# Optimization experiments

Measured on AMD Instinct MI355X. Metric: run time of the kernel, lower is better.

Reference implementation:

```python
import jax, jax.numpy as jnp
import numpy as np

B, N, M, K = 4, 2048, 8192, 3          # batches, coarse pts/batch, fine pts/batch, knn k
C_IN, C_SKIP, H, C_OUT = 256, 128, 256, 128


def setup_inputs() -> dict:
    key = jax.random.key(0)
    ks = jax.random.split(key, 8)
    x = jax.random.normal(ks[0], (B * N, C_IN), jnp.float32)
    pos = jax.random.normal(ks[1], (B * N, 3), jnp.float32)
    batch = jnp.repeat(jnp.arange(B, dtype=jnp.int64), N)        # sorted, equal-sized batches
    x_skip = jax.random.normal(ks[2], (B * M, C_SKIP), jnp.float32)
    pos_skip = jax.random.normal(ks[3], (B * M, 3), jnp.float32)
    batch_skip = jnp.repeat(jnp.arange(B, dtype=jnp.int64), M)
    # MLP params: Linear(384->256) + ReLU + Linear(256->128)
    W1 = jax.random.normal(ks[4], (C_IN + C_SKIP, H), jnp.float32) / np.sqrt(C_IN + C_SKIP)
    b1 = jnp.zeros((H,), jnp.float32)
    W2 = jax.random.normal(ks[5], (H, C_OUT), jnp.float32) / np.sqrt(H)
    b2 = jnp.zeros((C_OUT,), jnp.float32)
    return {"x": x, "pos": pos, "x_skip": x_skip, "pos_skip": pos_skip,
            "W1": W1, "b1": b1, "W2": W2, "b2": b2,
            "batch": batch, "batch_skip": batch_skip}


def _knn_interpolate(x, pos, pos_skip):
    # x: [B*N, C], pos: [B*N, 3], pos_skip: [B*M, 3]; batches are equal-sized & sorted,
    # so per-batch kNN == reshape to [B, n, ...] (matches batch/batch_skip vectors).
    xb = x.reshape(B, N, C_IN)
    pb = pos.reshape(B, N, 3)
    qb = pos_skip.reshape(B, M, 3)
    # squared pairwise distances via GEMM expansion: [B, M, N]
    d2 = (jnp.sum(qb * qb, -1)[:, :, None]
          + jnp.sum(pb * pb, -1)[:, None, :]
          - 2.0 * jnp.einsum('bmd,bnd->bmn', qb, pb))
    neg_d2, idx = jax.lax.top_k(-d2, K)           # k smallest distances
    d2k = jnp.maximum(-neg_d2, 0.0)               # [B, M, K]
    w = 1.0 / (d2k + 1e-16)                       # inverse-squared-distance weights
    feats = xb[jnp.arange(B)[:, None, None], idx] # gather: [B, M, K, C]
    interp = jnp.sum(w[..., None] * feats, axis=2) / jnp.sum(w, axis=2)[..., None]
    return interp.reshape(B * M, C_IN)


def reference(x, pos, x_skip, pos_skip, W1, b1, W2, b2, batch, batch_skip):
    xi = _knn_interpolate(x, pos, pos_skip)              # [B*M, C_IN]
    h = jnp.concatenate([xi, x_skip], axis=1)            # [B*M, C_IN+C_SKIP]
    h = jax.nn.relu(h @ W1 + b1)
    out = h @ W2 + b2                                    # [B*M, C_OUT]
    return (out, pos_skip, batch_skip)
```

## Files before the change

kernel.cpp:

```cpp
#include <hip/hip_runtime.h>
#include <math.h>
#include <stdint.h>

#define Bn    4
#define Nn    2048
#define Mn    8192
#define CIN   256
#define CSKIP 128
#define HID   256
#define COUT  128
#define KTOT  384

typedef short bf16x8 __attribute__((ext_vector_type(8)));
typedef float f32x16 __attribute__((ext_vector_type(16)));

__device__ __forceinline__ ushort f2bf(float f) {
    union { float f; unsigned u; } v; v.f = f;
    return (ushort)((v.u + 0x7fffu + ((v.u >> 16) & 1u)) >> 16);
}

__global__ __launch_bounds__(256) void fused_front(
    const float* __restrict__ x,
    const float* __restrict__ pos,
    const float* __restrict__ xs,
    const float* __restrict__ pos_skip,
    const float* __restrict__ W1, const float* __restrict__ W2,
    ushort* __restrict__ Abig,
    ushort* __restrict__ W1T, ushort* __restrict__ W2T,
    float* __restrict__ tail_dst)
{
    __shared__ float4 spos[Nn];
    __shared__ float  sPd[8][3][33];
    __shared__ int    sPi[8][3][33];
    __shared__ int    sIdx[32][3];
    __shared__ float  sW[32][4];

    const int bid = blockIdx.x;
    const int tid = threadIdx.x;

    if (bid >= 1024) {
        const int cb = bid - 1024;
        if (cb < 4096) {
            const int q   = cb * 256 + tid;
            const int row = q >> 5;
            const int cq  = (q & 31) * 4;
            const float4 v = *(const float4*)(xs + (size_t)row * CSKIP + cq);
            ushort4 o; o.x = f2bf(v.x); o.y = f2bf(v.y); o.z = f2bf(v.z); o.w = f2bf(v.w);
            *(ushort4*)(Abig + (size_t)row * KTOT + CIN + cq) = o;
        } else if (cb < 4192) {
            const int q  = (cb - 4096) * 256 + tid;
            const int n  = q / 96;
            const int kq = (q % 96) * 4;
            ushort4 o;
            o.x = f2bf(W1[(size_t)(kq + 0) * HID + n]);
            o.y = f2bf(W1[(size_t)(kq + 1) * HID + n]);
            o.z = f2bf(W1[(size_t)(kq + 2) * HID + n]);
            o.w = f2bf(W1[(size_t)(kq + 3) * HID + n]);
            *(ushort4*)(W1T + (size_t)n * KTOT + kq) = o;
        } else if (cb < 4224) {
            const int q  = (cb - 4192) * 256 + tid;
            const int n  = q >> 6;
            const int kq = (q & 63) * 4;
            ushort4 o;
            o.x = f2bf(W2[(size_t)(kq + 0) * COUT + n]);
            o.y = f2bf(W2[(size_t)(kq + 1) * COUT + n]);
            o.z = f2bf(W2[(size_t)(kq + 2) * COUT + n]);
            o.w = f2bf(W2[(size_t)(kq + 3) * COUT + n]);
            *(ushort4*)(W2T + (size_t)n * HID + kq) = o;
        } else {
            const int i = (cb - 4224) * 256 + tid;
            const int nPos = Bn * Mn * 3;
            if (i < nPos) tail_dst[i] = pos_skip[i];
            else          tail_dst[i] = (float)((i - nPos) >> 13);
        }
        return;
    }

    const int qloc   = tid & 31;
    const int chunk  = tid >> 5;
    const int blockQ = bid * 32;
    const int b      = blockQ / Mn;

    for (int i = tid; i < Nn; i += 256) {
        const float* p = pos + (size_t)(b * Nn + i) * 3;
        float p0 = p[0], p1 = p[1], p2 = p[2];
        float pp = __fadd_rn(__fadd_rn(__fmul_rn(p0, p0), __fmul_rn(p1, p1)),
                             __fmul_rn(p2, p2));
        spos[i] = make_float4(2.0f * p0, 2.0f * p1, 2.0f * p2, pp);
    }
    __syncthreads();

    const int q = blockQ + qloc;
    const float* qp = pos_skip + (size_t)q * 3;
    const float q0 = qp[0], q1 = qp[1], q2 = qp[2];
    const float qq = __fadd_rn(__fadd_rn(__fmul_rn(q0, q0), __fmul_rn(q1, q1)),
                               __fmul_rn(q2, q2));

    float dA = INFINITY, dB = INFINITY, dC = INFINITY;
    int   iA = 0, iB = 0, iC = 0;
    const int base = chunk * 256;
#pragma unroll 8
    for (int j = 0; j < 256; ++j) {
        const float4 P = spos[base + j];
        const float dot2 = __fadd_rn(__fadd_rn(__fmul_rn(q0, P.x), __fmul_rn(q1, P.y)),
                                     __fmul_rn(q2, P.z));
        const float d = __fsub_rn(__fadd_rn(qq, P.w), dot2);
        const int idx = base + j;
        const bool c1 = d < dA, c2 = d < dB, c3 = d < dC;
        dC = c3 ? (c2 ? dB : d) : dC;  iC = c3 ? (c2 ? iB : idx) : iC;
        dB = c2 ? (c1 ? dA : d) : dB;  iB = c2 ? (c1 ? iA : idx) : iB;
        dA = c1 ? d : dA;              iA = c1 ? idx : iA;
    }
    sPd[chunk][0][qloc] = dA; sPd[chunk][1][qloc] = dB; sPd[chunk][2][qloc] = dC;
    sPi[chunk][0][qloc] = iA; sPi[chunk][1][qloc] = iB; sPi[chunk][2][qloc] = iC;
    __syncthreads();

    if (tid < 32) {
        float mA = INFINITY, mB = INFINITY, mC = INFINITY;
        int   jA = 0, jB = 0, jC = 0;
#pragma unroll
        for (int c = 0; c < 8; ++c) {
#pragma unroll
            for (int s = 0; s < 3; ++s) {
                const float d = sPd[c][s][tid];
                const int   i = sPi[c][s][tid];
                const bool c1 = d < mA, c2 = d < mB, c3 = d < mC;
                mC = c3 ? (c2 ? mB : d) : mC;  jC = c3 ? (c2 ? jB : i) : jC;
                mB = c2 ? (c1 ? mA : d) : mB;  jB = c2 ? (c1 ? jA : i) : jB;
                mA = c1 ? d : mA;              jA = c1 ? i : jA;
            }
        }
        const float w0 = 1.0f / (fmaxf(mA, 0.0f) + 1e-16f);
        const float w1 = 1.0f / (fmaxf(mB, 0.0f) + 1e-16f);
        const float w2 = 1.0f / (fmaxf(mC, 0.0f) + 1e-16f);
        sIdx[tid][0] = jA; sIdx[tid][1] = jB; sIdx[tid][2] = jC;
        sW[tid][0] = w0; sW[tid][1] = w1; sW[tid][2] = w2;
        sW[tid][3] = w0 + w1 + w2;
    }
    __syncthreads();

    const int wave = tid >> 6, lane = tid & 63;
    const size_t xbase = (size_t)b * Nn * CIN;
    for (int j = 0; j < 8; ++j) {
        const int lq = wave * 8 + j;
        const int gq = blockQ + lq;
        const int i0 = sIdx[lq][0], i1 = sIdx[lq][1], i2 = sIdx[lq][2];
        const float w0 = sW[lq][0], w1 = sW[lq][1], w2 = sW[lq][2], den = sW[lq][3];
        const float4 f0 = ((const float4*)(x + xbase + (size_t)i0 * CIN))[lane];
        const float4 f1 = ((const float4*)(x + xbase + (size_t)i1 * CIN))[lane];
        const float4 f2 = ((const float4*)(x + xbase + (size_t)i2 * CIN))[lane];
        ushort4 ov;
        ov.x = f2bf((w0 * f0.x + w1 * f1.x + w2 * f2.x) / den);
        ov.y = f2bf((w0 * f0.y + w1 * f1.y + w2 * f2.y) / den);
        ov.z = f2bf((w0 * f0.z + w1 * f1.z + w2 * f2.z) / den);
        ov.w = f2bf((w0 * f0.w + w1 * f1.w + w2 * f2.w) / den);
        *(ushort4*)(Abig + (size_t)gq * KTOT + lane * 4) = ov;
    }
}

__global__ __launch_bounds__(256, 1) void mlp_fused(
    const ushort* __restrict__ Abig,
    const ushort* __restrict__ W1T,
    const float*  __restrict__ b1,
    const ushort* __restrict__ W2T,
    const float*  __restrict__ b2,
    float* __restrict__ out)
{
    __shared__ ushort Ast[128 * 32];
    __shared__ ushort Bst[128 * 32];
    __shared__ ushort Hs [128 * 128];

    const int tid  = threadIdx.x;
    const int wave = tid >> 6, lane = tid & 63;
    const int wr = wave >> 1, wc = wave & 1;
    const int l31 = lane & 31, kc0 = lane >> 5;
    const long rowbase = (long)blockIdx.x * 128;

    const int sr0 = tid >> 2;
    const int ss0 = tid & 3;
    const int ssw = (ss0 ^ (sr0 & 3));

    f32x16 acc2[2][2];
#pragma unroll
    for (int i = 0; i < 2; ++i)
#pragma unroll
        for (int j = 0; j < 2; ++j)
#pragma unroll
            for (int e = 0; e < 16; ++e) acc2[i][j][e] = 0.0f;

    for (int nh = 0; nh < 2; ++nh) {
        f32x16 acc1[2][2];
#pragma unroll
        for (int i = 0; i < 2; ++i)
#pragma unroll
            for (int j = 0; j < 2; ++j)
#pragma unroll
                for (int e = 0; e < 16; ++e) acc1[i][j][e] = 0.0f;

        const ushort* Ab = Abig + (size_t)rowbase * KTOT;
        const ushort* Wb = W1T + (size_t)(nh * 128) * KTOT;

        uint4 ra0, ra1, rb0, rb1;
        ra0 = *(const uint4*)(Ab + (size_t)sr0 * KTOT + ss0 * 8);
        ra1 = *(const uint4*)(Ab + (size_t)(sr0 + 64) * KTOT + ss0 * 8);
        rb0 = *(const uint4*)(Wb + (size_t)sr0 * KTOT + ss0 * 8);
        rb1 = *(const uint4*)(Wb + (size_t)(sr0 + 64) * KTOT + ss0 * 8);

        for (int t = 0; t < 12; ++t) {
            __syncthreads();
            *(uint4*)&Ast[sr0 * 32 + (ssw << 3)]        = ra0;
            *(uint4*)&Ast[(sr0 + 64) * 32 + (ssw << 3)] = ra1;
            *(uint4*)&Bst[sr0 * 32 + (ssw << 3)]        = rb0;
            *(uint4*)&Bst[(sr0 + 64) * 32 + (ssw << 3)] = rb1;
            __syncthreads();
            if (t < 11) {
                const int kt = (t + 1) * 32;
                ra0 = *(const uint4*)(Ab + (size_t)sr0 * KTOT + kt + ss0 * 8);
                ra1 = *(const uint4*)(Ab + (size_t)(sr0 + 64) * KTOT + kt + ss0 * 8);
                rb0 = *(const uint4*)(Wb + (size_t)sr0 * KTOT + kt + ss0 * 8);
                rb1 = *(const uint4*)(Wb + (size_t)(sr0 + 64) * KTOT + kt + ss0 * 8);
            }
#pragma unroll
            for (int s = 0; s < 2; ++s) {
                bf16x8 af[2], bq[2];
#pragma unroll
                for (int mf = 0; mf < 2; ++mf) {
                    const int r = wr * 64 + mf * 32 + l31;
                    af[mf] = *(const bf16x8*)&Ast[r * 32 + ((((s << 1) | kc0) ^ (r & 3)) << 3)];
                }
#pragma unroll
                for (int nf = 0; nf < 2; ++nf) {
                    const int rn = wc * 64 + nf * 32 + l31;
                    bq[nf] = *(const bf16x8*)&Bst[rn * 32 + ((((s << 1) | kc0) ^ (rn & 3)) << 3)];
                }
#pragma unroll
                for (int mf = 0; mf < 2; ++mf)
#pragma unroll
                    for (int nf = 0; nf < 2; ++nf)
                        acc1[mf][nf] = __builtin_amdgcn_mfma_f32_32x32x16_bf16(
                            af[mf], bq[nf], acc1[mf][nf], 0, 0, 0);
            }
        }

#pragma unroll
        for (int mf = 0; mf < 2; ++mf)
#pragma unroll
            for (int nf = 0; nf < 2; ++nf) {
                const int col = wc * 64 + nf * 32 + l31;
                const float b1v = b1[nh * 128 + col];
#pragma unroll
                for (int e = 0; e < 16; ++e) {
                    const int rl = wr * 64 + mf * 32 + (e & 3) + ((e >> 2) << 3) + (kc0 << 2);
                    const float hv = fmaxf(acc1[mf][nf][e] + b1v, 0.0f);
                    Hs[rl * 128 + (((col >> 3) ^ (rl & 7)) << 3) + (col & 7)] = f2bf(hv);
                }
            }
        __syncthreads();

        uint4 rw0, rw1;
        rw0 = *(const uint4*)(W2T + (size_t)sr0 * HID + nh * 128 + ss0 * 8);
        rw1 = *(const uint4*)(W2T + (size_t)(sr0 + 64) * HID + nh * 128 + ss0 * 8);

        for (int t = 0; t < 4; ++t) {
            __syncthreads();
            *(uint4*)&Bst[sr0 * 32 + (ssw << 3)]        = rw0;
            *(uint4*)&Bst[(sr0 + 64) * 32 + (ssw << 3)] = rw1;
            __syncthreads();
            if (t < 3) {
                const int kt = nh * 128 + (t + 1) * 32;
                rw0 = *(const uint4*)(W2T + (size_t)sr0 * HID + kt + ss0 * 8);
                rw1 = *(const uint4*)(W2T + (size_t)(sr0 + 64) * HID + kt + ss0 * 8);
            }
#pragma unroll
            for (int s = 0; s < 2; ++s) {
                bf16x8 af[2], bq[2];
#pragma unroll
                for (int mf = 0; mf < 2; ++mf) {
                    const int r  = wr * 64 + mf * 32 + l31;
                    const int kc = (t << 2) + (s << 1) + kc0;
                    af[mf] = *(const bf16x8*)&Hs[r * 128 + ((kc ^ (r & 7)) << 3)];
                }
#pragma unroll
                for (int nf = 0; nf < 2; ++nf) {
                    const int rn = wc * 64 + nf * 32 + l31;
                    bq[nf] = *(const bf16x8*)&Bst[rn * 32 + ((((s << 1) | kc0) ^ (rn & 3)) << 3)];
                }
#pragma unroll
                for (int mf = 0; mf < 2; ++mf)
#pragma unroll
                    for (int nf = 0; nf < 2; ++nf)
                        acc2[mf][nf] = __builtin_amdgcn_mfma_f32_32x32x16_bf16(
                            af[mf], bq[nf], acc2[mf][nf], 0, 0, 0);
            }
        }
        __syncthreads();
    }

#pragma unroll
    for (int mf = 0; mf < 2; ++mf)
#pragma unroll
        for (int nf = 0; nf < 2; ++nf) {
            const int col = wc * 64 + nf * 32 + l31;
            const float b2v = b2[col];
#pragma unroll
            for (int e = 0; e < 16; ++e) {
                const int rl = wr * 64 + mf * 32 + (e & 3) + ((e >> 2) << 3) + (kc0 << 2);
                out[(rowbase + rl) * COUT + col] = acc2[mf][nf][e] + b2v;
            }
        }
}

extern "C" void kernel_launch(void* const* d_in, const int* in_sizes, int n_in,
                              void* d_out, int out_size, void* d_ws, size_t ws_size,
                              hipStream_t stream)
{
    const float* x        = (const float*)d_in[0];
    const float* pos      = (const float*)d_in[1];
    const float* x_skip   = (const float*)d_in[2];
    const float* pos_skip = (const float*)d_in[3];
    const float* W1       = (const float*)d_in[4];
    const float* b1       = (const float*)d_in[5];
    const float* W2       = (const float*)d_in[6];
    const float* b2       = (const float*)d_in[7];

    float* out = (float*)d_out;

    ushort* Abig = (ushort*)d_ws;
    ushort* W1T  = (ushort*)((char*)d_ws + (size_t)Bn * Mn * KTOT * 2);
    ushort* W2T  = (ushort*)((char*)W1T + (size_t)HID * KTOT * 2);

    fused_front<<<dim3(1024 + 4224 + 512), 256, 0, stream>>>(
        x, pos, x_skip, pos_skip, W1, W2, Abig, W1T, W2T,
        out + (size_t)Bn * Mn * COUT);

    mlp_fused<<<dim3(Bn * Mn / 128), 256, 0, stream>>>(
        Abig, W1T, b1, W2T, b2, out);
}
```

Measured before the change: 77.23 us.

## Use two-pass kNN: med3 value-only top-3 then thresholded index pass

```diff
diff --git a/kernel.cpp b/kernel.cpp
--- a/kernel.cpp
+++ b/kernel.cpp
@@ -32,6 +32,7 @@
     __shared__ float4 spos[Nn];
     __shared__ float  sPd[8][3][33];
     __shared__ int    sPi[8][3][33];
+    __shared__ float  sG[33];
     __shared__ int    sIdx[32][3];
     __shared__ float  sW[32][4];
 
@@ -95,41 +96,79 @@
     const float q0 = qp[0], q1 = qp[1], q2 = qp[2];
     const float qq = __fadd_rn(__fadd_rn(__fmul_rn(q0, q0), __fmul_rn(q1, q1)),
                                __fmul_rn(q2, q2));
-
-    float dA = INFINITY, dB = INFINITY, dC = INFINITY;
-    int   iA = 0, iB = 0, iC = 0;
     const int base = chunk * 256;
+
+    {
+        float v1 = INFINITY, v2 = INFINITY, v3 = INFINITY;
 #pragma unroll 8
-    for (int j = 0; j < 256; ++j) {
-        const float4 P = spos[base + j];
-        const float dot2 = __fadd_rn(__fadd_rn(__fmul_rn(q0, P.x), __fmul_rn(q1, P.y)),
-                                     __fmul_rn(q2, P.z));
-        const float d = __fsub_rn(__fadd_rn(qq, P.w), dot2);
-        const int idx = base + j;
-        const bool c1 = d < dA, c2 = d < dB, c3 = d < dC;
-        dC = c3 ? (c2 ? dB : d) : dC;  iC = c3 ? (c2 ? iB : idx) : iC;
-        dB = c2 ? (c1 ? dA : d) : dB;  iB = c2 ? (c1 ? iA : idx) : iB;
-        dA = c1 ? d : dA;              iA = c1 ? idx : iA;
-    }
-    sPd[chunk][0][qloc] = dA; sPd[chunk][1][qloc] = dB; sPd[chunk][2][qloc] = dC;
-    sPi[chunk][0][qloc] = iA; sPi[chunk][1][qloc] = iB; sPi[chunk][2][qloc] = iC;
+        for (int j = 0; j < 256; ++j) {
+            const float4 P = spos[base + j];
+            const float dot2 = __fadd_rn(__fadd_rn(__fmul_rn(q0, P.x), __fmul_rn(q1, P.y)),
+                                         __fmul_rn(q2, P.z));
+            const float d = __fsub_rn(__fadd_rn(qq, P.w), dot2);
+            v3 = __builtin_amdgcn_fmed3f(d, v2, v3);
+            v2 = __builtin_amdgcn_fmed3f(d, v1, v2);
+            v1 = fminf(v1, d);
+        }
+        sPd[chunk][0][qloc] = v1; sPd[chunk][1][qloc] = v2; sPd[chunk][2][qloc] = v3;
+    }
+    __syncthreads();
+
+    if (tid < 32) {
+        float g1 = INFINITY, g2 = INFINITY, g3 = INFINITY;
+#pragma unroll
+        for (int c = 0; c < 8; ++c)
+#pragma unroll
+            for (int s = 0; s < 3; ++s) {
+                const float d = sPd[c][s][tid];
+                g3 = __builtin_amdgcn_fmed3f(d, g2, g3);
+                g2 = __builtin_amdgcn_fmed3f(d, g1, g2);
+                g1 = fminf(g1, d);
+            }
+        sG[tid] = g3;
+    }
+    __syncthreads();
+
+    {
+        const float g3 = sG[qloc];
+        float md0 = INFINITY, md1 = INFINITY, md2 = INFINITY;
+        int   mi0 = 0, mi1 = 0, mi2 = 0;
+#pragma unroll 4
+        for (int j = 0; j < 256; ++j) {
+            const float4 P = spos[base + j];
+            const float dot2 = __fadd_rn(__fadd_rn(__fmul_rn(q0, P.x), __fmul_rn(q1, P.y)),
+                                         __fmul_rn(q2, P.z));
+            const float d = __fsub_rn(__fadd_rn(qq, P.w), dot2);
+            if (d <= g3) {
+                const int idx = base + j;
+                const bool c1 = d < md0, c2 = d < md1, c3 = d < md2;
+                md2 = c3 ? (c2 ? md1 : d) : md2;  mi2 = c3 ? (c2 ? mi1 : idx) : mi2;
+                md1 = c2 ? (c1 ? md0 : d) : md1;  mi1 = c2 ? (c1 ? mi0 : idx) : mi1;
+                md0 = c1 ? d : md0;               mi0 = c1 ? idx : mi0;
+            }
+        }
+        __syncthreads();
+        sPd[chunk][0][qloc] = md0; sPd[chunk][1][qloc] = md1; sPd[chunk][2][qloc] = md2;
+        sPi[chunk][0][qloc] = mi0; sPi[chunk][1][qloc] = mi1; sPi[chunk][2][qloc] = mi2;
+    }
     __syncthreads();
 
     if (tid < 32) {
         float mA = INFINITY, mB = INFINITY, mC = INFINITY;
-        int   jA = 0, jB = 0, jC = 0;
-#pragma unroll
-        for (int c = 0; c < 8; ++c) {
+        int   jA = 0x7fffffff, jB = 0x7fffffff, jC = 0x7fffffff;
+#pragma unroll
+        for (int c = 0; c < 8; ++c)
 #pragma unroll
             for (int s = 0; s < 3; ++s) {
                 const float d = sPd[c][s][tid];
                 const int   i = sPi[c][s][tid];
-                const bool c1 = d < mA, c2 = d < mB, c3 = d < mC;
-                mC = c3 ? (c2 ? mB : d) : mC;  jC = c3 ? (c2 ? jB : i) : jC;
-                mB = c2 ? (c1 ? mA : d) : mB;  jB = c2 ? (c1 ? jA : i) : jB;
-                mA = c1 ? d : mA;              jA = c1 ? i : jA;
-            }
-        }
+                const bool b1 = (d < mA) || (d == mA && i < jA);
+                const bool b2 = (d < mB) || (d == mB && i < jB);
+                const bool b3 = (d < mC) || (d == mC && i < jC);
+                mC = b3 ? (b2 ? mB : d) : mC;  jC = b3 ? (b2 ? jB : i) : jC;
+                mB = b2 ? (b1 ? mA : d) : mB;  jB = b2 ? (b1 ? jA : i) : jB;
+                mA = b1 ? d : mA;              jA = b1 ? i : jA;
+            }
         const float w0 = 1.0f / (fmaxf(mA, 0.0f) + 1e-16f);
         const float w1 = 1.0f / (fmaxf(mB, 0.0f) + 1e-16f);
         const float w2 = 1.0f / (fmaxf(mC, 0.0f) + 1e-16f);
```

Measured after the change: 84.33 us. +9.2%, slower.

## Precompute packed positions in separate kernel and halve queries per kNN block

Applied to the files above, without the earlier changes.

```diff
diff --git a/kernel.cpp b/kernel.cpp
--- a/kernel.cpp
+++ b/kernel.cpp
@@ -19,9 +19,20 @@
     return (ushort)((v.u + 0x7fffu + ((v.u >> 16) & 1u)) >> 16);
 }
 
-__global__ __launch_bounds__(256) void fused_front(
+__global__ __launch_bounds__(256) void pack_pos4(
+    const float* __restrict__ pos, float4* __restrict__ pos4)
+{
+    const int i = blockIdx.x * 256 + threadIdx.x;
+    const float* p = pos + (size_t)i * 3;
+    const float p0 = p[0], p1 = p[1], p2 = p[2];
+    const float pp = __fadd_rn(__fadd_rn(__fmul_rn(p0, p0), __fmul_rn(p1, p1)),
+                               __fmul_rn(p2, p2));
+    pos4[i] = make_float4(2.0f * p0, 2.0f * p1, 2.0f * p2, pp);
+}
+
+__global__ __launch_bounds__(256) void fused_mid(
     const float* __restrict__ x,
-    const float* __restrict__ pos,
+    const float4* __restrict__ pos4,
     const float* __restrict__ xs,
     const float* __restrict__ pos_skip,
     const float* __restrict__ W1, const float* __restrict__ W2,
@@ -29,17 +40,16 @@
     ushort* __restrict__ W1T, ushort* __restrict__ W2T,
     float* __restrict__ tail_dst)
 {
-    __shared__ float4 spos[Nn];
-    __shared__ float  sPd[8][3][33];
-    __shared__ int    sPi[8][3][33];
-    __shared__ int    sIdx[32][3];
-    __shared__ float  sW[32][4];
+    __shared__ float sPd[16][3][17];
+    __shared__ int   sPi[16][3][17];
+    __shared__ int   sIdx[16][3];
+    __shared__ float sW[16][4];
 
     const int bid = blockIdx.x;
     const int tid = threadIdx.x;
 
-    if (bid >= 1024) {
-        const int cb = bid - 1024;
+    if (bid >= 2048) {
+        const int cb = bid - 2048;
         if (cb < 4096) {
             const int q   = cb * 256 + tid;
             const int row = q >> 5;
@@ -76,19 +86,10 @@
         return;
     }
 
-    const int qloc   = tid & 31;
-    const int chunk  = tid >> 5;
-    const int blockQ = bid * 32;
+    const int qloc   = tid & 15;
+    const int chunk  = tid >> 4;
+    const int blockQ = bid * 16;
     const int b      = blockQ / Mn;
-
-    for (int i = tid; i < Nn; i += 256) {
-        const float* p = pos + (size_t)(b * Nn + i) * 3;
-        float p0 = p[0], p1 = p[1], p2 = p[2];
-        float pp = __fadd_rn(__fadd_rn(__fmul_rn(p0, p0), __fmul_rn(p1, p1)),
-                             __fmul_rn(p2, p2));
-        spos[i] = make_float4(2.0f * p0, 2.0f * p1, 2.0f * p2, pp);
-    }
-    __syncthreads();
 
     const int q = blockQ + qloc;
     const float* qp = pos_skip + (size_t)q * 3;
@@ -96,12 +97,14 @@
     const float qq = __fadd_rn(__fadd_rn(__fmul_rn(q0, q0), __fmul_rn(q1, q1)),
                                __fmul_rn(q2, q2));
 
+    const int base = chunk * 128;
+    const float4* __restrict__ cp = pos4 + (size_t)b * Nn + base;
+
     float dA = INFINITY, dB = INFINITY, dC = INFINITY;
     int   iA = 0, iB = 0, iC = 0;
-    const int base = chunk * 256;
-#pragma unroll 8
-    for (int j = 0; j < 256; ++j) {
-        const float4 P = spos[base + j];
+#pragma unroll 4
+    for (int j = 0; j < 128; ++j) {
+        const float4 P = cp[j];
         const float dot2 = __fadd_rn(__fadd_rn(__fmul_rn(q0, P.x), __fmul_rn(q1, P.y)),
                                      __fmul_rn(q2, P.z));
         const float d = __fsub_rn(__fadd_rn(qq, P.w), dot2);
@@ -115,11 +118,11 @@
     sPi[chunk][0][qloc] = iA; sPi[chunk][1][qloc] = iB; sPi[chunk][2][qloc] = iC;
     __syncthreads();
 
-    if (tid < 32) {
+    if (tid < 16) {
         float mA = INFINITY, mB = INFINITY, mC = INFINITY;
         int   jA = 0, jB = 0, jC = 0;
 #pragma unroll
-        for (int c = 0; c < 8; ++c) {
+        for (int c = 0; c < 16; ++c)
 #pragma unroll
             for (int s = 0; s < 3; ++s) {
                 const float d = sPd[c][s][tid];
@@ -129,7 +132,6 @@
                 mB = c2 ? (c1 ? mA : d) : mB;  jB = c2 ? (c1 ? jA : i) : jB;
                 mA = c1 ? d : mA;              jA = c1 ? i : jA;
             }
-        }
         const float w0 = 1.0f / (fmaxf(mA, 0.0f) + 1e-16f);
         const float w1 = 1.0f / (fmaxf(mB, 0.0f) + 1e-16f);
         const float w2 = 1.0f / (fmaxf(mC, 0.0f) + 1e-16f);
@@ -141,8 +143,8 @@
 
     const int wave = tid >> 6, lane = tid & 63;
     const size_t xbase = (size_t)b * Nn * CIN;
-    for (int j = 0; j < 8; ++j) {
-        const int lq = wave * 8 + j;
+    for (int j = 0; j < 4; ++j) {
+        const int lq = wave * 4 + j;
         const int gq = blockQ + lq;
         const int i0 = sIdx[lq][0], i1 = sIdx[lq][1], i2 = sIdx[lq][2];
         const float w0 = sW[lq][0], w1 = sW[lq][1], w2 = sW[lq][2], den = sW[lq][3];
@@ -328,9 +330,12 @@
     ushort* Abig = (ushort*)d_ws;
     ushort* W1T  = (ushort*)((char*)d_ws + (size_t)Bn * Mn * KTOT * 2);
     ushort* W2T  = (ushort*)((char*)W1T + (size_t)HID * KTOT * 2);
-
-    fused_front<<<dim3(1024 + 4224 + 512), 256, 0, stream>>>(
-        x, pos, x_skip, pos_skip, W1, W2, Abig, W1T, W2T,
+    float4* pos4 = (float4*)((char*)W2T + (size_t)COUT * HID * 2);
+
+    pack_pos4<<<dim3(Bn * Nn / 256), 256, 0, stream>>>(pos, pos4);
+
+    fused_mid<<<dim3(2048 + 4736), 256, 0, stream>>>(
+        x, pos4, x_skip, pos_skip, W1, W2, Abig, W1T, W2T,
         out + (size_t)Bn * Mn * COUT);
 
     mlp_fused<<<dim3(Bn * Mn / 128), 256, 0, stream>>>(
```

Measured after the change: 82.51 us. +6.8%, slower.
